# Optimization experiments

Hardware: AMD Instinct MI355X
Metric: run time of the kernel (lower is better)

The kernel has to match this reference:

```python
import jax, jax.numpy as jnp
import numpy as np

N, E, H, C, IN = 20000, 640000, 4, 64, 256
HC = H * C
NEG_SLOPE = 0.2


def setup_inputs() -> dict:
    key = jax.random.key(0)
    ks = jax.random.split(key, 24)
    rn = lambda k, s: jax.random.normal(k, s, jnp.float32) * 0.05
    return {
        "x": jax.random.normal(ks[0], (N, IN), jnp.float32),
        "edge_index": jax.random.randint(ks[1], (2, E), 0, N),
        "confidence": jax.random.normal(ks[2], (N,), jnp.float32),
        "w_in": rn(ks[3], (IN, C)), "b_in": jnp.zeros((C,), jnp.float32),
        "lin_w0": rn(ks[4], (C, HC)),
        "lin_w12": rn(ks[5], (2, HC, HC)),
        "att_src": rn(ks[6], (3, H, C)),
        "att_dst": rn(ks[7], (3, H, C)),
        "gat_bias": jnp.zeros((3, HC), jnp.float32),
        "conf_w": rn(ks[8], (HC, 1)), "conf_b": jnp.zeros((1,), jnp.float32),
        "nc_w1": rn(ks[9], (HC, C)), "nc_b1": jnp.zeros((C,), jnp.float32),
        "nc_w2": rn(ks[10], (C, 1)), "nc_b2": jnp.zeros((1,), jnp.float32),
        "oc_w1": rn(ks[11], (HC, C)), "oc_b1": jnp.zeros((C,), jnp.float32),
        "oc_w2": rn(ks[12], (C, 1)), "oc_b2": jnp.zeros((1,), jnp.float32),
        "ec_w1": rn(ks[13], (HC, C)), "ec_b1": jnp.zeros((C,), jnp.float32),
        "ec_w2": rn(ks[14], (C, 4)), "ec_b2": jnp.zeros((4,), jnp.float32),
    }


def _gat_layer(h_in, src, dst, n, lin_w, a_src, a_dst, bias):
    # h_in: (n, in_ch). PyG GATConv: linear -> per-edge attn -> segment softmax -> scatter-add.
    h = (h_in @ lin_w).reshape(n, H, C)
    s_src = jnp.einsum("nhc,hc->nh", h, a_src)  # (n, H)
    s_dst = jnp.einsum("nhc,hc->nh", h, a_dst)
    alpha = jax.nn.leaky_relu(s_src[src] + s_dst[dst], NEG_SLOPE)  # (E', H)
    # softmax over incoming edges of each dst node (self-loops guarantee coverage)
    amax = jax.ops.segment_max(alpha, dst, num_segments=n)
    ex = jnp.exp(alpha - amax[dst])
    denom = jax.ops.segment_sum(ex, dst, num_segments=n)
    coef = ex / jnp.maximum(denom[dst], 1e-16)
    msg = h[src] * coef[:, :, None]  # (E', H, C)
    out = jax.ops.segment_sum(msg, dst, num_segments=n)
    return out.reshape(n, HC) + bias


def reference(x, edge_index, confidence, w_in, b_in, lin_w0, lin_w12,
              att_src, att_dst, gat_bias, conf_w, conf_b,
              nc_w1, nc_b1, nc_w2, nc_b2, oc_w1, oc_b1, oc_w2, oc_b2,
              ec_w1, ec_b1, ec_w2, ec_b2):
    n = x.shape[0]
    loops = jnp.arange(n)
    src = jnp.concatenate([edge_index[0], loops])  # PyG add_self_loops=True
    dst = jnp.concatenate([edge_index[1], loops])
    h = jax.nn.relu(x @ w_in + b_in)  # input_proj + relu (dropout off in eval)
    lin_ws = [lin_w0, lin_w12[0], lin_w12[1]]
    conf_norm = jax.nn.sigmoid(confidence)  # (n,)
    for i in range(3):
        h_new = _gat_layer(h, src, dst, n, lin_ws[i], att_src[i], att_dst[i], gat_bias[i])
        cw = jax.nn.sigmoid(h_new @ conf_w + conf_b)[:, 0] * conf_norm
        h_new = h_new * cw[:, None]
        h = h + h_new if h.shape[-1] == h_new.shape[-1] else h_new
        if i < 2:
            h = jax.nn.relu(h)
    mlp = lambda w1, b1, w2, b2: jax.nn.relu(h @ w1 + b1) @ w2 + b2
    node_pred = jax.nn.sigmoid(mlp(nc_w1, nc_b1, nc_w2, nc_b2))[:, 0]
    origin_pred = jax.nn.sigmoid(mlp(oc_w1, oc_b1, oc_w2, oc_b2))[:, 0]
    error_type_pred = mlp(ec_w1, ec_b1, ec_w2, ec_b2)
    return node_pred, origin_pred, error_type_pred, h
```

## Files before the change

kernel.cpp:

```cpp
#include <hip/hip_runtime.h>
#include <cstdint>
#include <cstddef>

#define NN   20000
#define NPAD 20224
#define EE   640000
#define E2   660000
#define HHD  4
#define CC   64
#define HC   256
#define NEG  0.2f

#define NBUK 313
#define NBLK 129
#define EPB  5120
#define SCN  (NBUK * NBLK)
#define PREP_BLKS 5000
#define GEMM_BLKS (NPAD / 64)

typedef short bf16x8 __attribute__((ext_vector_type(8)));
typedef float f32x4 __attribute__((ext_vector_type(4)));

__device__ __forceinline__ float sigmoidf_(float x) { return 1.0f / (1.0f + __expf(-x)); }

__device__ __forceinline__ float wred_sum(float v) {
#pragma unroll
    for (int d = 32; d; d >>= 1) v += __shfl_xor(v, d, 64);
    return v;
}

__device__ __forceinline__ unsigned short f2bf(float f) {
    unsigned u = __float_as_uint(f);
    u = (u + 0x7fff + ((u >> 16) & 1)) >> 16;
    return (unsigned short)u;
}
__device__ __forceinline__ float bfval(unsigned short h) { return __uint_as_float(((unsigned)h) << 16); }
__device__ __forceinline__ float bf_lo(unsigned u) { return __uint_as_float(u << 16); }
__device__ __forceinline__ float bf_hi(unsigned u) { return __uint_as_float(u & 0xffff0000u); }


__device__ __forceinline__ void hist_body(int bl, const int* __restrict__ ei,
                                          int* __restrict__ bhist, int* h ) {
    int t = threadIdx.x;
    for (int i = t; i < NBUK; i += 256) h[i] = 0;
    __syncthreads();
    int e0 = bl * EPB;
#pragma unroll 4
    for (int i = t; i < EPB; i += 256) {
        int e = e0 + i;
        if (e < E2) {
            int d = (e < EE) ? ei[EE + e] : (e - EE);
            atomicAdd(&h[d >> 6], 1);
        }
    }
    __syncthreads();
    for (int i = t; i < NBUK; i += 256) bhist[i * NBLK + bl] = h[i];
}

__device__ __forceinline__ void scatter_body(int bl, const int* __restrict__ ei,
                                             const int* __restrict__ sbase,
                                             unsigned int* __restrict__ ebuf,
                                             int* cur ) {
    int t = threadIdx.x;
    for (int i = t; i < NBUK; i += 256) cur[i] = sbase[i * NBLK + bl];
    __syncthreads();
    int e0 = bl * EPB;
#pragma unroll 4
    for (int i = t; i < EPB; i += 256) {
        int e = e0 + i;
        if (e < E2) {
            int s, d;
            if (e < EE) { s = ei[e]; d = ei[EE + e]; }
            else        { s = e - EE; d = s; }
            int p = atomicAdd(&cur[d >> 6], 1);
            ebuf[p] = ((unsigned int)(d & 63) << 15) | (unsigned int)s;
        }
    }
}

__device__ __forceinline__ void build_body(int bu, const unsigned int* __restrict__ ebuf,
                                           const int* __restrict__ sbase,
                                           int* __restrict__ off, int* __restrict__ csr,
                                           int* hist ) {
    int* sc = hist + 64;
    int* curl = hist + 128;
    int t = threadIdx.x;
    int base = sbase[bu * NBLK];
    int end  = (bu + 1 < NBUK) ? sbase[(bu + 1) * NBLK] : E2;
    int ne = end - base;
    if (t < 64) hist[t] = 0;
    __syncthreads();
    for (int i = t; i < ne; i += 256) {
        int dl = (int)(ebuf[base + i] >> 15);
        atomicAdd(&hist[dl], 1);
    }
    __syncthreads();
    if (t < 64) sc[t] = hist[t];
    __syncthreads();
    for (int d = 1; d < 64; d <<= 1) {
        int v = (t < 64 && t >= d) ? sc[t - d] : 0;
        __syncthreads();
        if (t < 64) sc[t] += v;
        __syncthreads();
    }
    int n0 = bu * 64;
    if (t < 64) {
        int ex = base + sc[t] - hist[t];
        if (n0 + t < NN) off[n0 + t] = ex;
        curl[t] = ex;
    }
    if (bu == NBUK - 1 && t == 0) off[NN] = E2;
    __syncthreads();
    for (int i = t; i < ne; i += 256) {
        unsigned int v = ebuf[base + i];
        int dl = (int)(v >> 15);
        int p = atomicAdd(&curl[dl], 1);
        csr[p] = (int)(v & 0x7fffu);
    }
}

#define WTOT 212992
__device__ __forceinline__ void prep_body(int idx,
                            const float* __restrict__ x,
                            const float* __restrict__ w_in, const float* __restrict__ lin_w0,
                            const float* __restrict__ lin_w12,
                            const float* __restrict__ nc1, const float* __restrict__ oc1,
                            const float* __restrict__ ec1,
                            const float* __restrict__ nb, const float* __restrict__ ob,
                            const float* __restrict__ eb,
                            unsigned short* __restrict__ whi,
                            float* __restrict__ bcat,
                            unsigned short* __restrict__ xh, unsigned short* __restrict__ xl) {
    if (idx < NN * 64) {
        float4 v = ((const float4*)x)[idx];
        ushort4 hi, lo;
        hi.x = f2bf(v.x); lo.x = f2bf(v.x - bfval(hi.x));
        hi.y = f2bf(v.y); lo.y = f2bf(v.y - bfval(hi.y));
        hi.z = f2bf(v.z); lo.z = f2bf(v.z - bfval(hi.z));
        hi.w = f2bf(v.w); lo.w = f2bf(v.w - bfval(hi.w));
        ((ushort4*)xh)[idx] = hi;
        ((ushort4*)xl)[idx] = lo;
    }
    if (idx < 192) {
        int g = idx >> 6, jj = idx & 63;
        const float* b = (g == 0) ? nb : ((g == 1) ? ob : eb);
        bcat[idx] = b[jj];
    }
    if (idx >= WTOT) return;
    float v;
    if (idx < 16384) {
        int n = idx >> 8, k = idx & 255;
        v = w_in[k * 64 + n];
    } else if (idx < 32768) {
        int r = idx - 16384;
        int n = r >> 6, k = r & 63;
        v = lin_w0[k * 256 + n];
    } else if (idx < 98304) {
        int r = idx - 32768;
        int n = r >> 8, k = r & 255;
        v = lin_w12[k * 256 + n];
    } else if (idx < 163840) {
        int r = idx - 98304;
        int n = r >> 8, k = r & 255;
        v = lin_w12[65536 + k * 256 + n];
    } else {
        int r = idx - 163840;
        int n = r >> 8, k = r & 255;
        int g = n >> 6, jj = n & 63;
        const float* w = (g == 0) ? nc1 : ((g == 1) ? oc1 : ec1);
        v = w[k * 64 + jj];
    }
    whi[idx] = f2bf(v);
}

template <int K, int OUT_CH, int MODE, int NT>
__device__ __forceinline__ void gemm_body(
    unsigned short* Bh,
    int mb,
    const unsigned short* __restrict__ Ahp, const unsigned short* __restrict__ Alp,
    const unsigned short* __restrict__ Wh,
    const float* __restrict__ bias,
    unsigned short* __restrict__ Outh,
    const float* __restrict__ a_src, const float* __restrict__ a_dst,
    float* __restrict__ s_src, float* __restrict__ s_dst,
    const float* __restrict__ w2n, const float* __restrict__ w2o,
    const float* __restrict__ w2e,
    const float* __restrict__ b2n, const float* __restrict__ b2o,
    const float* __restrict__ b2e,
    unsigned short* __restrict__ Outl,
    float* __restrict__ outbuf, int nreal) {
    constexpr int LB = K + 8;
    constexpr int NS = K / 32;
    const int tid = threadIdx.x;
    const int wv = tid >> 6, lane = tid & 63;
    const int quad = lane >> 4, ln = lane & 15;
    const int r0 = mb + wv * 16 + ln;

    const unsigned short* aph = Ahp + (size_t)r0 * K + quad * 8;
    const unsigned short* apl = Alp + (size_t)r0 * K + quad * 8;
    bf16x8 ah[NS], al[NS];
#pragma unroll
    for (int s = 0; s < NS; s++) {
        ah[s] = *(const bf16x8*)(aph + s * 32);
        al[s] = *(const bf16x8*)(apl + s * 32);
    }

    for (int ct = 0; ct < NT; ct++) {
        const int cb = ct * 64;
        if (ct > 0) __syncthreads();

        constexpr int NCHK = 64 * (K / 8);
#pragma unroll
        for (int i = 0; i < NCHK / 256; i++) {
            int flat = tid + i * 256;
            int r = flat / (K / 8);
            int c = (flat % (K / 8)) * 8;
            *(uint4*)&Bh[r * LB + c] = *(const uint4*)&Wh[(size_t)(cb + r) * K + c];
        }
        __syncthreads();

        f32x4 acc[4];
#pragma unroll
        for (int j = 0; j < 4; j++) {
            acc[j][0] = 0.f; acc[j][1] = 0.f; acc[j][2] = 0.f; acc[j][3] = 0.f;
        }

#pragma unroll
        for (int s = 0; s < NS; s++) {
#pragma unroll
            for (int cg = 0; cg < 4; cg++) {
                bf16x8 bh = *(const bf16x8*)&Bh[(cg * 16 + ln) * LB + quad * 8 + s * 32];
                acc[cg] = __builtin_amdgcn_mfma_f32_16x16x32_bf16(ah[s], bh, acc[cg], 0, 0, 0);
                acc[cg] = __builtin_amdgcn_mfma_f32_16x16x32_bf16(al[s], bh, acc[cg], 0, 0, 0);
            }
        }

        if (MODE == 1) {
            float av[4], dv[4];
#pragma unroll
            for (int cg = 0; cg < 4; cg++) {
                av[cg] = a_src[cb + cg * 16 + ln];
                dv[cg] = a_dst[cb + cg * 16 + ln];
            }
#pragma unroll
            for (int reg = 0; reg < 4; reg++) {
                float ps = 0.f, pd = 0.f;
#pragma unroll
                for (int cg = 0; cg < 4; cg++) {
                    float t = acc[cg][reg];
                    ps += t * av[cg];
                    pd += t * dv[cg];
                }
#pragma unroll
                for (int d = 1; d < 16; d <<= 1) {
                    ps += __shfl_xor(ps, d, 64);
                    pd += __shfl_xor(pd, d, 64);
                }
                if (ln == 0) {
                    int row = mb + wv * 16 + quad * 4 + reg;
                    if (row < nreal) {
                        s_src[row * 4 + ct] = ps;
                        s_dst[row * 4 + ct] = pd;
                    }
                }
            }
        }

        if (MODE == 3) {
            float bv[4];
#pragma unroll
            for (int cg = 0; cg < 4; cg++) bv[cg] = bias[cb + cg * 16 + ln];
            if (ct < 2) {
                const float* w2 = (ct == 0) ? w2n : w2o;
                float b2 = (ct == 0) ? b2n[0] : b2o[0];
                float wv2[4];
#pragma unroll
                for (int cg = 0; cg < 4; cg++) wv2[cg] = w2[cg * 16 + ln];
#pragma unroll
                for (int reg = 0; reg < 4; reg++) {
                    float t = 0.f;
#pragma unroll
                    for (int cg = 0; cg < 4; cg++) {
                        float tv = fmaxf(acc[cg][reg] + bv[cg], 0.f);
                        t += tv * wv2[cg];
                    }
#pragma unroll
                    for (int d = 1; d < 16; d <<= 1) t += __shfl_xor(t, d, 64);
                    int row = mb + wv * 16 + quad * 4 + reg;
                    if (ln == 0 && row < nreal)
                        outbuf[ct * NN + row] = sigmoidf_(t + b2);
                }
            } else {
                float4 w4[4];
#pragma unroll
                for (int cg = 0; cg < 4; cg++) w4[cg] = ((const float4*)w2e)[cg * 16 + ln];
#pragma unroll
                for (int reg = 0; reg < 4; reg++) {
                    float e0 = 0.f, e1 = 0.f, e2 = 0.f, e3 = 0.f;
#pragma unroll
                    for (int cg = 0; cg < 4; cg++) {
                        float tv = fmaxf(acc[cg][reg] + bv[cg], 0.f);
                        e0 += tv * w4[cg].x; e1 += tv * w4[cg].y;
                        e2 += tv * w4[cg].z; e3 += tv * w4[cg].w;
                    }
#pragma unroll
                    for (int d = 1; d < 16; d <<= 1) {
                        e0 += __shfl_xor(e0, d, 64); e1 += __shfl_xor(e1, d, 64);
                        e2 += __shfl_xor(e2, d, 64); e3 += __shfl_xor(e3, d, 64);
                    }
                    int row = mb + wv * 16 + quad * 4 + reg;
                    if (ln == 0 && row < nreal) {
                        float4 ev = make_float4(e0 + b2e[0], e1 + b2e[1], e2 + b2e[2], e3 + b2e[3]);
                        *(float4*)&outbuf[2 * NN + row * 4] = ev;
                    }
                }
            }
            continue;
        }

#pragma unroll
        for (int cg = 0; cg < 4; cg++) {
            int col = cb + cg * 16 + ln;
            int rbase = mb + wv * 16 + quad * 4;
#pragma unroll
            for (int reg = 0; reg < 4; reg++) {
                float v = acc[cg][reg];
                int r = rbase + reg;
                if (MODE == 0) {
                    v += bias[col]; v = fmaxf(v, 0.f);
                    unsigned short hi = f2bf(v);
                    Outh[(size_t)r * OUT_CH + col] = hi;
                    Outl[(size_t)r * OUT_CH + col] = f2bf(v - bfval(hi));
                } else if (MODE == 1) {
                    Outh[(size_t)r * OUT_CH + col] = f2bf(v);
                }
            }
        }
    }
}


__global__ __launch_bounds__(256) void prep_hist(
    const float* __restrict__ x,
    const float* __restrict__ w_in, const float* __restrict__ lin_w0,
    const float* __restrict__ lin_w12,
    const float* __restrict__ nc1, const float* __restrict__ oc1,
    const float* __restrict__ ec1,
    const float* __restrict__ nb, const float* __restrict__ ob,
    const float* __restrict__ eb,
    unsigned short* __restrict__ whi, float* __restrict__ bcat,
    unsigned short* __restrict__ xh, unsigned short* __restrict__ xl,
    const int* __restrict__ ei, int* __restrict__ bhist) {
    __shared__ int h[NBUK];
    if (blockIdx.x < PREP_BLKS) {
        prep_body(blockIdx.x * 256 + threadIdx.x, x, w_in, lin_w0, lin_w12,
                  nc1, oc1, ec1, nb, ob, eb, whi, bcat, xh, xl);
    } else {
        hist_body(blockIdx.x - PREP_BLKS, ei, bhist, h);
    }
}

__global__ __launch_bounds__(1024) void scan_hist(const int* __restrict__ bhist,
                                                  int* __restrict__ sbase) {
    __shared__ int buf[1024];
    int t = threadIdx.x;
    int base = t * 40;
    int local[40];
    int s = 0;
#pragma unroll
    for (int i = 0; i < 40; i++) {
        int idx = base + i;
        int v = (idx < SCN) ? bhist[idx] : 0;
        local[i] = v;
        s += v;
    }
    buf[t] = s;
    __syncthreads();
    for (int d = 1; d < 1024; d <<= 1) {
        int tv = (t >= d) ? buf[t - d] : 0;
        __syncthreads();
        buf[t] += tv;
        __syncthreads();
    }
    int run = buf[t] - s;
#pragma unroll
    for (int i = 0; i < 40; i++) {
        int idx = base + i;
        if (idx < SCN) sbase[idx] = run;
        run += local[i];
    }
}

__global__ __launch_bounds__(256) void scatter_proj(
    const int* __restrict__ ei, const int* __restrict__ sbase,
    unsigned int* __restrict__ ebuf,
    const unsigned short* __restrict__ xh, const unsigned short* __restrict__ xl,
    const unsigned short* __restrict__ wt_in, const float* __restrict__ b_in,
    unsigned short* __restrict__ h0h, unsigned short* __restrict__ h0l) {
    __shared__ unsigned short smem[64 * (256 + 8)];
    if (blockIdx.x < NBLK) {
        scatter_body(blockIdx.x, ei, sbase, ebuf, (int*)smem);
    } else {
        gemm_body<256, 64, 0, 1>(smem, (int)(blockIdx.x - NBLK) * 64,
                                 xh, xl, wt_in, b_in, h0h,
                                 nullptr, nullptr, nullptr, nullptr,
                                 nullptr, nullptr, nullptr, nullptr, nullptr, nullptr,
                                 h0l, nullptr, NN);
    }
}

__global__ __launch_bounds__(256) void build_l0(
    const unsigned int* __restrict__ ebuf, const int* __restrict__ sbase,
    int* __restrict__ off, int* __restrict__ csr,
    const unsigned short* __restrict__ h0h, const unsigned short* __restrict__ h0l,
    const unsigned short* __restrict__ wt_l0,
    unsigned short* __restrict__ hh,
    const float* __restrict__ a_src, const float* __restrict__ a_dst,
    float* __restrict__ ssrc, float* __restrict__ sdst) {
    __shared__ unsigned short smem[64 * (64 + 8)];
    if (blockIdx.x < NBUK) {
        build_body(blockIdx.x, ebuf, sbase, off, csr, (int*)smem);
    } else {
        gemm_body<64, 256, 1, 4>(smem, (int)(blockIdx.x - NBUK) * 64,
                                 h0h, h0l, wt_l0, nullptr, hh,
                                 a_src, a_dst, ssrc, sdst,
                                 nullptr, nullptr, nullptr, nullptr, nullptr, nullptr,
                                 nullptr, nullptr, NN);
    }
}

template <int K, int OUT_CH, int MODE, int NT>
__global__ __launch_bounds__(256) void gemm_lds(
    const unsigned short* __restrict__ Ahp, const unsigned short* __restrict__ Alp,
    const unsigned short* __restrict__ Wh,
    const float* __restrict__ bias,
    unsigned short* __restrict__ Outh, unsigned short* __restrict__ Outl,
    const float* __restrict__ a_src, const float* __restrict__ a_dst,
    float* __restrict__ s_src, float* __restrict__ s_dst,
    const float* __restrict__ w2n, const float* __restrict__ w2o,
    const float* __restrict__ w2e,
    const float* __restrict__ b2n, const float* __restrict__ b2o,
    const float* __restrict__ b2e,
    float* __restrict__ outbuf, int nreal) {
    __shared__ unsigned short Bh[64 * (K + 8)];
    gemm_body<K, OUT_CH, MODE, NT>(Bh, blockIdx.x * 64, Ahp, Alp, Wh, bias, Outh,
                                   a_src, a_dst, s_src, s_dst,
                                   w2n, w2o, w2e, b2n, b2o, b2e, Outl, outbuf, nreal);
}

__global__ __launch_bounds__(256) void gat_node(const unsigned short* __restrict__ hhb,
                                                const float* __restrict__ s_src,
                                                const float* __restrict__ s_dst,
                                                const int* __restrict__ csr_src,
                                                const int* __restrict__ csr_off,
                                                const float* __restrict__ gbias,
                                                const float* __restrict__ conf_w,
                                                const float* __restrict__ conf_b,
                                                const float* __restrict__ confid,
                                                unsigned short* __restrict__ h_hi,
                                                unsigned short* __restrict__ h_lo,
                                                float* __restrict__ outbuf,
                                                int layer) {
    __shared__ float Lc[4][64];
    __shared__ int   Ls[4][16];
    int wv = threadIdx.x >> 6;
    int lane = threadIdx.x & 63;
    int n = blockIdx.x * 4 + wv;
    int myhead = lane >> 4, slot = lane & 15;
    int off0 = csr_off[n];
    int deg = csr_off[n + 1] - off0;
    const int* cp = csr_src + off0;
    const unsigned short* hrow = hhb + lane * 4;
    float sdm = s_dst[n * 4 + myhead];

    float ax = 0.f, ay = 0.f, az = 0.f, aw = 0.f, smp = 0.f;
    int nch = (deg + 15) >> 4;
    bool valid = slot < deg;
    int sl = cp[valid ? slot : deg - 1];
    float ssv = s_src[sl * 4 + myhead];
    for (int t = 0; t < nch; t++) {
        float a = ssv + sdm;
        a = a > 0.f ? a : NEG * a;
        float c = valid ? __expf(a) : 0.f;
        smp += c;
        Lc[wv][lane] = c;
        if (myhead == 0) Ls[wv][slot] = sl;
        __builtin_amdgcn_wave_barrier();
        float4 c0 = *(const float4*)&Lc[wv][myhead * 16 + 0];
        float4 c1 = *(const float4*)&Lc[wv][myhead * 16 + 4];
        float4 c2 = *(const float4*)&Lc[wv][myhead * 16 + 8];
        float4 c3 = *(const float4*)&Lc[wv][myhead * 16 + 12];
        int4 s0 = *(const int4*)&Ls[wv][0];
        int4 s1 = *(const int4*)&Ls[wv][4];
        int4 s2 = *(const int4*)&Ls[wv][8];
        int4 s3 = *(const int4*)&Ls[wv][12];
        __builtin_amdgcn_wave_barrier();
        if (t + 1 < nch) {
            int i = ((t + 1) << 4) + slot;
            valid = i < deg;
            sl = cp[valid ? i : deg - 1];
            ssv = s_src[sl * 4 + myhead];
        }
        float cf[16] = {c0.x, c0.y, c0.z, c0.w, c1.x, c1.y, c1.z, c1.w,
                        c2.x, c2.y, c2.z, c2.w, c3.x, c3.y, c3.z, c3.w};
        int sv[16] = {s0.x, s0.y, s0.z, s0.w, s1.x, s1.y, s1.z, s1.w,
                      s2.x, s2.y, s2.z, s2.w, s3.x, s3.y, s3.z, s3.w};
#pragma unroll
        for (int q = 0; q < 16; q++) {
            uint2 u = *(const uint2*)(hrow + ((size_t)sv[q] << 8));
            ax += cf[q] * bf_lo(u.x); ay += cf[q] * bf_hi(u.x);
            az += cf[q] * bf_lo(u.y); aw += cf[q] * bf_hi(u.y);
        }
    }
    smp += __shfl_xor(smp, 1, 64);
    smp += __shfl_xor(smp, 2, 64);
    smp += __shfl_xor(smp, 4, 64);
    smp += __shfl_xor(smp, 8, 64);
    float inv = 1.0f / fmaxf(smp, 1e-16f);
    ax *= inv; ay *= inv; az *= inv; aw *= inv;

    float4 b4 = *(const float4*)&gbias[lane * 4];
    float hx = ax + b4.x, hy = ay + b4.y, hz = az + b4.z, hw = aw + b4.w;
    float4 cw4 = *(const float4*)&conf_w[lane * 4];
    float local = hx * cw4.x + hy * cw4.y + hz * cw4.z + hw * cw4.w;
    float tot = wred_sum(local);
    float cw = sigmoidf_(tot + conf_b[0]) * sigmoidf_(confid[n]);
    hx *= cw; hy *= cw; hz *= cw; hw *= cw;
    if (layer > 0) {
        ushort4 ph = *(const ushort4*)&h_hi[(size_t)n * HC + lane * 4];
        ushort4 pl = *(const ushort4*)&h_lo[(size_t)n * HC + lane * 4];
        hx += bfval(ph.x) + bfval(pl.x);
        hy += bfval(ph.y) + bfval(pl.y);
        hz += bfval(ph.z) + bfval(pl.z);
        hw += bfval(ph.w) + bfval(pl.w);
    }
    if (layer < 2) {
        hx = fmaxf(hx, 0.f); hy = fmaxf(hy, 0.f);
        hz = fmaxf(hz, 0.f); hw = fmaxf(hw, 0.f);
    } else {
        *(float4*)&outbuf[6 * NN + (size_t)n * HC + lane * 4] =
            make_float4(hx, hy, hz, hw);
    }
    ushort4 oh, ol;
    oh.x = f2bf(hx); ol.x = f2bf(hx - bfval(oh.x));
    oh.y = f2bf(hy); ol.y = f2bf(hy - bfval(oh.y));
    oh.z = f2bf(hz); ol.z = f2bf(hz - bfval(oh.z));
    oh.w = f2bf(hw); ol.w = f2bf(hw - bfval(oh.w));
    *(ushort4*)&h_hi[(size_t)n * HC + lane * 4] = oh;
    *(ushort4*)&h_lo[(size_t)n * HC + lane * 4] = ol;
}

extern "C" void kernel_launch(void* const* d_in, const int* in_sizes, int n_in,
                              void* d_out, int out_size, void* d_ws, size_t ws_size,
                              hipStream_t stream) {
    const float* x       = (const float*)d_in[0];
    const int*   ei      = (const int*)d_in[1];
    const float* conf    = (const float*)d_in[2];
    const float* w_in    = (const float*)d_in[3];
    const float* b_in    = (const float*)d_in[4];
    const float* lin_w0  = (const float*)d_in[5];
    const float* lin_w12 = (const float*)d_in[6];
    const float* att_src = (const float*)d_in[7];
    const float* att_dst = (const float*)d_in[8];
    const float* gbias   = (const float*)d_in[9];
    const float* conf_w  = (const float*)d_in[10];
    const float* conf_b  = (const float*)d_in[11];
    const float* nc_w1   = (const float*)d_in[12];
    const float* nc_b1   = (const float*)d_in[13];
    const float* nc_w2   = (const float*)d_in[14];
    const float* nc_b2   = (const float*)d_in[15];
    const float* oc_w1   = (const float*)d_in[16];
    const float* oc_b1   = (const float*)d_in[17];
    const float* oc_w2   = (const float*)d_in[18];
    const float* oc_b2   = (const float*)d_in[19];
    const float* ec_w1   = (const float*)d_in[20];
    const float* ec_b1   = (const float*)d_in[21];
    const float* ec_w2   = (const float*)d_in[22];
    const float* ec_b2   = (const float*)d_in[23];
    float* out = (float*)d_out;

    char* p = (char*)d_ws;
    auto alloc = [&](size_t bytes) -> void* {
        void* r = (void*)p;
        p += (bytes + 255) & ~(size_t)255;
        return r;
    };
    unsigned short* h_hi = (unsigned short*)alloc((size_t)NPAD * HC * 2);
    unsigned short* h_lo = (unsigned short*)alloc((size_t)NPAD * HC * 2);
    unsigned short* hh   = (unsigned short*)alloc((size_t)NPAD * HC * 2);
    unsigned short* h0h  = (unsigned short*)alloc((size_t)NPAD * CC * 2);
    unsigned short* h0l  = (unsigned short*)alloc((size_t)NPAD * CC * 2);
    float*          ssrc = (float*)alloc((size_t)NN * 4 * 4);
    float*          sdst = (float*)alloc((size_t)NN * 4 * 4);
    int*            off  = (int*)alloc((size_t)(NN + 1) * 4);
    int*            csr  = (int*)alloc((size_t)E2 * 4);
    int*            bhist= (int*)alloc((size_t)SCN * 4);
    int*            sbase= (int*)alloc((size_t)SCN * 4);
    unsigned int*   ebuf = (unsigned int*)alloc((size_t)E2 * 4);
    unsigned short* whi  = (unsigned short*)alloc((size_t)WTOT * 2);
    float*          bcat = (float*)alloc((size_t)192 * 4);
    unsigned short* xh   = (unsigned short*)alloc((size_t)NPAD * 256 * 2 * 2);
    unsigned short* xl   = xh + (size_t)NPAD * 256;

    const unsigned short* wt_in = whi;
    const unsigned short* wt_l0 = whi + 16384;
    const unsigned short* wt_a  = whi + 32768;
    const unsigned short* wt_b  = whi + 98304;
    const unsigned short* wt_hd = whi + 163840;

    prep_hist<<<PREP_BLKS + NBLK, 256, 0, stream>>>(
        x, w_in, lin_w0, lin_w12, nc_w1, oc_w1, ec_w1, nc_b1, oc_b1, ec_b1,
        whi, bcat, xh, xl, ei, bhist);

    scan_hist<<<1, 1024, 0, stream>>>(bhist, sbase);

    scatter_proj<<<NBLK + GEMM_BLKS, 256, 0, stream>>>(
        ei, sbase, ebuf, xh, xl, wt_in, b_in, h0h, h0l);

    build_l0<<<NBUK + GEMM_BLKS, 256, 0, stream>>>(
        ebuf, sbase, off, csr, h0h, h0l, wt_l0, hh, att_src, att_dst, ssrc, sdst);

    gat_node<<<NN / 4, 256, 0, stream>>>(hh, ssrc, sdst, csr, off, gbias, conf_w, conf_b, conf,
                                         h_hi, h_lo, out, 0);

    for (int i = 1; i < 3; i++) {
        const unsigned short* wh = (i == 1) ? wt_a : wt_b;
        gemm_lds<256, 256, 1, 4><<<dim3(GEMM_BLKS, 1), 256, 0, stream>>>(
            h_hi, h_lo, wh, nullptr, hh, nullptr,
            att_src + i * HHD * CC, att_dst + i * HHD * CC, ssrc, sdst,
            nullptr, nullptr, nullptr, nullptr, nullptr, nullptr, nullptr, NN);
        gat_node<<<NN / 4, 256, 0, stream>>>(hh, ssrc, sdst, csr, off, gbias + i * HC,
                                             conf_w, conf_b, conf, h_hi, h_lo, out, i);
    }

    gemm_lds<256, 192, 3, 3><<<dim3(GEMM_BLKS, 1), 256, 0, stream>>>(
        h_hi, h_lo, wt_hd, bcat, nullptr, nullptr, nullptr, nullptr, nullptr, nullptr,
        nc_w2, oc_w2, ec_w2, nc_b2, oc_b2, ec_b2, out, NN);
}
```

Measured before the change: 370.8 us.

## Split GAT aggregation into per-head kernel plus finalize kernel

Replaces the per-node GAT aggregation kernel with a per-(node, head) kernel. In it, each wave processes one head's 64 channels with 8 edges in parallel and 16-byte gathers. Partial aggregates and per-head confidence dot products go to new float buffers, and a second kernel applies the confidence gate, residual and bf16 split. The aim is more parallelism and wider gathers without LDS staging. The cost is an extra fp32 round trip through global memory of N×256 floats per layer and an extra launch. Grid blocks are interleaved so heads of nearby nodes run close together.

Result: slower. 435.9 us (+17.6%).

```diff
diff --git a/kernel.cpp b/kernel.cpp
--- a/kernel.cpp
+++ b/kernel.cpp
@@ -22,12 +22,6 @@
 typedef float f32x4 __attribute__((ext_vector_type(4)));
 
 __device__ __forceinline__ float sigmoidf_(float x) { return 1.0f / (1.0f + __expf(-x)); }
-
-__device__ __forceinline__ float wred_sum(float v) {
-#pragma unroll
-    for (int d = 32; d; d >>= 1) v += __shfl_xor(v, d, 64);
-    return v;
-}
 
 __device__ __forceinline__ unsigned short f2bf(float f) {
     unsigned u = __float_as_uint(f);
@@ -448,84 +442,92 @@
                                    w2n, w2o, w2e, b2n, b2o, b2e, Outl, outbuf, nreal);
 }
 
-__global__ __launch_bounds__(256) void gat_node(const unsigned short* __restrict__ hhb,
-                                                const float* __restrict__ s_src,
-                                                const float* __restrict__ s_dst,
-                                                const int* __restrict__ csr_src,
-                                                const int* __restrict__ csr_off,
-                                                const float* __restrict__ gbias,
-                                                const float* __restrict__ conf_w,
-                                                const float* __restrict__ conf_b,
-                                                const float* __restrict__ confid,
-                                                unsigned short* __restrict__ h_hi,
-                                                unsigned short* __restrict__ h_lo,
-                                                float* __restrict__ outbuf,
-                                                int layer) {
-    __shared__ float Lc[4][64];
-    __shared__ int   Ls[4][16];
+__global__ __launch_bounds__(256) void gat_head(
+    const unsigned short* __restrict__ hhb,
+    const float* __restrict__ s_src, const float* __restrict__ s_dst,
+    const int* __restrict__ csr_src, const int* __restrict__ csr_off,
+    const float* __restrict__ gbias, const float* __restrict__ conf_w,
+    float* __restrict__ agg, float* __restrict__ pdot) {
+    int bid = blockIdx.x;
+    int h  = (bid & 7) >> 1;
+    int ng = ((bid >> 3) << 1) | (bid & 1);
     int wv = threadIdx.x >> 6;
     int lane = threadIdx.x & 63;
-    int n = blockIdx.x * 4 + wv;
-    int myhead = lane >> 4, slot = lane & 15;
+    int n = ng * 4 + wv;
+    int slot = lane >> 3;
+    int oct  = lane & 7;
     int off0 = csr_off[n];
-    int deg = csr_off[n + 1] - off0;
+    int deg  = csr_off[n + 1] - off0;
     const int* cp = csr_src + off0;
-    const unsigned short* hrow = hhb + lane * 4;
-    float sdm = s_dst[n * 4 + myhead];
-
-    float ax = 0.f, ay = 0.f, az = 0.f, aw = 0.f, smp = 0.f;
-    int nch = (deg + 15) >> 4;
+    const unsigned short* hrow = hhb + h * 64 + oct * 8;
+    float sdm = s_dst[n * 4 + h];
+
+    float ac[8] = {0.f, 0.f, 0.f, 0.f, 0.f, 0.f, 0.f, 0.f};
+    float smp = 0.f;
+    int nch = (deg + 7) >> 3;
     bool valid = slot < deg;
     int sl = cp[valid ? slot : deg - 1];
-    float ssv = s_src[sl * 4 + myhead];
+    float ssv = s_src[sl * 4 + h];
     for (int t = 0; t < nch; t++) {
         float a = ssv + sdm;
         a = a > 0.f ? a : NEG * a;
         float c = valid ? __expf(a) : 0.f;
         smp += c;
-        Lc[wv][lane] = c;
-        if (myhead == 0) Ls[wv][slot] = sl;
-        __builtin_amdgcn_wave_barrier();
-        float4 c0 = *(const float4*)&Lc[wv][myhead * 16 + 0];
-        float4 c1 = *(const float4*)&Lc[wv][myhead * 16 + 4];
-        float4 c2 = *(const float4*)&Lc[wv][myhead * 16 + 8];
-        float4 c3 = *(const float4*)&Lc[wv][myhead * 16 + 12];
-        int4 s0 = *(const int4*)&Ls[wv][0];
-        int4 s1 = *(const int4*)&Ls[wv][4];
-        int4 s2 = *(const int4*)&Ls[wv][8];
-        int4 s3 = *(const int4*)&Ls[wv][12];
-        __builtin_amdgcn_wave_barrier();
+        int cursl = sl;
         if (t + 1 < nch) {
-            int i = ((t + 1) << 4) + slot;
+            int i = ((t + 1) << 3) + slot;
             valid = i < deg;
             sl = cp[valid ? i : deg - 1];
-            ssv = s_src[sl * 4 + myhead];
-        }
-        float cf[16] = {c0.x, c0.y, c0.z, c0.w, c1.x, c1.y, c1.z, c1.w,
-                        c2.x, c2.y, c2.z, c2.w, c3.x, c3.y, c3.z, c3.w};
-        int sv[16] = {s0.x, s0.y, s0.z, s0.w, s1.x, s1.y, s1.z, s1.w,
-                      s2.x, s2.y, s2.z, s2.w, s3.x, s3.y, s3.z, s3.w};
-#pragma unroll
-        for (int q = 0; q < 16; q++) {
-            uint2 u = *(const uint2*)(hrow + ((size_t)sv[q] << 8));
-            ax += cf[q] * bf_lo(u.x); ay += cf[q] * bf_hi(u.x);
-            az += cf[q] * bf_lo(u.y); aw += cf[q] * bf_hi(u.y);
-        }
-    }
-    smp += __shfl_xor(smp, 1, 64);
-    smp += __shfl_xor(smp, 2, 64);
-    smp += __shfl_xor(smp, 4, 64);
+            ssv = s_src[sl * 4 + h];
+        }
+        uint4 u = *(const uint4*)(hrow + ((size_t)cursl << 8));
+        ac[0] += c * bf_lo(u.x); ac[1] += c * bf_hi(u.x);
+        ac[2] += c * bf_lo(u.y); ac[3] += c * bf_hi(u.y);
+        ac[4] += c * bf_lo(u.z); ac[5] += c * bf_hi(u.z);
+        ac[6] += c * bf_lo(u.w); ac[7] += c * bf_hi(u.w);
+    }
     smp += __shfl_xor(smp, 8, 64);
+    smp += __shfl_xor(smp, 16, 64);
+    smp += __shfl_xor(smp, 32, 64);
+#pragma unroll
+    for (int i = 0; i < 8; i++) {
+        ac[i] += __shfl_xor(ac[i], 8, 64);
+        ac[i] += __shfl_xor(ac[i], 16, 64);
+        ac[i] += __shfl_xor(ac[i], 32, 64);
+    }
     float inv = 1.0f / fmaxf(smp, 1e-16f);
-    ax *= inv; ay *= inv; az *= inv; aw *= inv;
-
-    float4 b4 = *(const float4*)&gbias[lane * 4];
-    float hx = ax + b4.x, hy = ay + b4.y, hz = az + b4.z, hw = aw + b4.w;
-    float4 cw4 = *(const float4*)&conf_w[lane * 4];
-    float local = hx * cw4.x + hy * cw4.y + hz * cw4.z + hw * cw4.w;
-    float tot = wred_sum(local);
+    int cbase = h * 64 + oct * 8;
+    float vv[8];
+    float pd = 0.f;
+#pragma unroll
+    for (int i = 0; i < 8; i++) {
+        vv[i] = ac[i] * inv + gbias[cbase + i];
+        pd += vv[i] * conf_w[cbase + i];
+    }
+    pd += __shfl_xor(pd, 1, 64);
+    pd += __shfl_xor(pd, 2, 64);
+    pd += __shfl_xor(pd, 4, 64);
+    if (lane < 8) {
+        float* ap = agg + (size_t)n * 256 + cbase;
+        *(float4*)ap       = make_float4(vv[0], vv[1], vv[2], vv[3]);
+        *(float4*)(ap + 4) = make_float4(vv[4], vv[5], vv[6], vv[7]);
+        if (lane == 0) pdot[n * 4 + h] = pd;
+    }
+}
+
+__global__ __launch_bounds__(256) void gat_fin(
+    const float* __restrict__ agg, const float* __restrict__ pdot,
+    const float* __restrict__ conf_b, const float* __restrict__ confid,
+    unsigned short* __restrict__ h_hi, unsigned short* __restrict__ h_lo,
+    float* __restrict__ outbuf, int layer) {
+    int wv = threadIdx.x >> 6;
+    int lane = threadIdx.x & 63;
+    int n = blockIdx.x * 4 + wv;
+    float4 v = *(const float4*)(agg + (size_t)n * 256 + lane * 4);
+    const float* pp = pdot + n * 4;
+    float tot = pp[0] + pp[1] + pp[2] + pp[3];
     float cw = sigmoidf_(tot + conf_b[0]) * sigmoidf_(confid[n]);
-    hx *= cw; hy *= cw; hz *= cw; hw *= cw;
+    float hx = v.x * cw, hy = v.y * cw, hz = v.z * cw, hw = v.w * cw;
     if (layer > 0) {
         ushort4 ph = *(const ushort4*)&h_hi[(size_t)n * HC + lane * 4];
         ushort4 pl = *(const ushort4*)&h_lo[(size_t)n * HC + lane * 4];
@@ -601,6 +603,8 @@
     float*          bcat = (float*)alloc((size_t)192 * 4);
     unsigned short* xh   = (unsigned short*)alloc((size_t)NPAD * 256 * 2 * 2);
     unsigned short* xl   = xh + (size_t)NPAD * 256;
+    float*          agg  = (float*)alloc((size_t)NN * 256 * 4);
+    float*          pdot = (float*)alloc((size_t)NN * 4 * 4);
 
     const unsigned short* wt_in = whi;
     const unsigned short* wt_l0 = whi + 16384;
@@ -620,8 +624,8 @@
     build_l0<<<NBUK + GEMM_BLKS, 256, 0, stream>>>(
         ebuf, sbase, off, csr, h0h, h0l, wt_l0, hh, att_src, att_dst, ssrc, sdst);
 
-    gat_node<<<NN / 4, 256, 0, stream>>>(hh, ssrc, sdst, csr, off, gbias, conf_w, conf_b, conf,
-                                         h_hi, h_lo, out, 0);
+    gat_head<<<NN, 256, 0, stream>>>(hh, ssrc, sdst, csr, off, gbias, conf_w, agg, pdot);
+    gat_fin<<<NN / 4, 256, 0, stream>>>(agg, pdot, conf_b, conf, h_hi, h_lo, out, 0);
 
     for (int i = 1; i < 3; i++) {
         const unsigned short* wh = (i == 1) ? wt_a : wt_b;
@@ -629,8 +633,9 @@
             h_hi, h_lo, wh, nullptr, hh, nullptr,
             att_src + i * HHD * CC, att_dst + i * HHD * CC, ssrc, sdst,
             nullptr, nullptr, nullptr, nullptr, nullptr, nullptr, nullptr, NN);
-        gat_node<<<NN / 4, 256, 0, stream>>>(hh, ssrc, sdst, csr, off, gbias + i * HC,
-                                             conf_w, conf_b, conf, h_hi, h_lo, out, i);
+        gat_head<<<NN, 256, 0, stream>>>(hh, ssrc, sdst, csr, off, gbias + i * HC,
+                                         conf_w, agg, pdot);
+        gat_fin<<<NN / 4, 256, 0, stream>>>(agg, pdot, conf_b, conf, h_hi, h_lo, out, i);
     }
 
     gemm_lds<256, 192, 3, 3><<<dim3(GEMM_BLKS, 1), 256, 0, stream>>>(
```

## Fold global histogram scan into scatter blocks and drop scan kernel launch

Applied to the files above, without the earlier changes.

Removes the single-block scan_hist kernel. Each scatter block now recomputes its own per-bucket prefix and the bucket totals straight from the histogram matrix, then scans the bucket totals in LDS to get its write cursors, with block 0 also writing compact bucket start offsets for the build step. This cuts one kernel launch and a serialized single-block stage, but every scatter block now reads the whole 313x129 histogram redundantly, with strided row reads.

After: 358.6 us. 3.3% less time.

```diff
diff --git a/kernel.cpp b/kernel.cpp
--- a/kernel.cpp
+++ b/kernel.cpp
@@ -14,7 +14,6 @@
 #define NBUK 313
 #define NBLK 129
 #define EPB  5120
-#define SCN  (NBUK * NBLK)
 #define PREP_BLKS 5000
 #define GEMM_BLKS (NPAD / 64)
 
@@ -58,35 +57,68 @@
 }
 
 __device__ __forceinline__ void scatter_body(int bl, const int* __restrict__ ei,
-                                             const int* __restrict__ sbase,
+                                             const int* __restrict__ bhist,
                                              unsigned int* __restrict__ ebuf,
-                                             int* cur ) {
+                                             int* __restrict__ bstart,
+                                             int* ih ) {
+    int* tot = ih;
+    int* par = ih + NBUK;
+    int* buf = ih + 2 * NBUK;
+    int* cur = ih + 2 * NBUK + 256;
     int t = threadIdx.x;
-    for (int i = t; i < NBUK; i += 256) cur[i] = sbase[i * NBLK + bl];
+    for (int i = t; i < NBUK; i += 256) {
+        const int* row = bhist + i * NBLK;
+        int sp = 0;
+        for (int b = 0; b < bl; b++) sp += row[b];
+        int st = sp;
+        for (int b = bl; b < NBLK; b++) st += row[b];
+        tot[i] = st; par[i] = sp;
+    }
+    __syncthreads();
+    int b0 = t * 2;
+    int v0 = (b0 < NBUK) ? tot[b0] : 0;
+    int v1 = (b0 + 1 < NBUK) ? tot[b0 + 1] : 0;
+    int s = v0 + v1;
+    buf[t] = s;
+    __syncthreads();
+    for (int d = 1; d < 256; d <<= 1) {
+        int tv = (t >= d) ? buf[t - d] : 0;
+        __syncthreads();
+        buf[t] += tv;
+        __syncthreads();
+    }
+    int excl = buf[t] - s;
+    if (b0 < NBUK)     cur[b0]     = excl + par[b0];
+    if (b0 + 1 < NBUK) cur[b0 + 1] = excl + v0 + par[b0 + 1];
+    if (bl == 0) {
+        if (b0 < NBUK)     bstart[b0]     = excl;
+        if (b0 + 1 < NBUK) bstart[b0 + 1] = excl + v0;
+        if (t == 0) bstart[NBUK] = E2;
+    }
     __syncthreads();
     int e0 = bl * EPB;
 #pragma unroll 4
     for (int i = t; i < EPB; i += 256) {
         int e = e0 + i;
         if (e < E2) {
-            int s, d;
-            if (e < EE) { s = ei[e]; d = ei[EE + e]; }
-            else        { s = e - EE; d = s; }
+            int s2, d;
+            if (e < EE) { s2 = ei[e]; d = ei[EE + e]; }
+            else        { s2 = e - EE; d = s2; }
             int p = atomicAdd(&cur[d >> 6], 1);
-            ebuf[p] = ((unsigned int)(d & 63) << 15) | (unsigned int)s;
+            ebuf[p] = ((unsigned int)(d & 63) << 15) | (unsigned int)s2;
         }
     }
 }
 
 __device__ __forceinline__ void build_body(int bu, const unsigned int* __restrict__ ebuf,
-                                           const int* __restrict__ sbase,
+                                           const int* __restrict__ bstart,
                                            int* __restrict__ off, int* __restrict__ csr,
                                            int* hist ) {
     int* sc = hist + 64;
     int* curl = hist + 128;
     int t = threadIdx.x;
-    int base = sbase[bu * NBLK];
-    int end  = (bu + 1 < NBUK) ? sbase[(bu + 1) * NBLK] : E2;
+    int base = bstart[bu];
+    int end  = bstart[bu + 1];
     int ne = end - base;
     if (t < 64) hist[t] = 0;
     __syncthreads();
@@ -360,46 +392,15 @@
     }
 }
 
-__global__ __launch_bounds__(1024) void scan_hist(const int* __restrict__ bhist,
-                                                  int* __restrict__ sbase) {
-    __shared__ int buf[1024];
-    int t = threadIdx.x;
-    int base = t * 40;
-    int local[40];
-    int s = 0;
-#pragma unroll
-    for (int i = 0; i < 40; i++) {
-        int idx = base + i;
-        int v = (idx < SCN) ? bhist[idx] : 0;
-        local[i] = v;
-        s += v;
-    }
-    buf[t] = s;
-    __syncthreads();
-    for (int d = 1; d < 1024; d <<= 1) {
-        int tv = (t >= d) ? buf[t - d] : 0;
-        __syncthreads();
-        buf[t] += tv;
-        __syncthreads();
-    }
-    int run = buf[t] - s;
-#pragma unroll
-    for (int i = 0; i < 40; i++) {
-        int idx = base + i;
-        if (idx < SCN) sbase[idx] = run;
-        run += local[i];
-    }
-}
-
 __global__ __launch_bounds__(256) void scatter_proj(
-    const int* __restrict__ ei, const int* __restrict__ sbase,
-    unsigned int* __restrict__ ebuf,
+    const int* __restrict__ ei, const int* __restrict__ bhist,
+    unsigned int* __restrict__ ebuf, int* __restrict__ bstart,
     const unsigned short* __restrict__ xh, const unsigned short* __restrict__ xl,
     const unsigned short* __restrict__ wt_in, const float* __restrict__ b_in,
     unsigned short* __restrict__ h0h, unsigned short* __restrict__ h0l) {
     __shared__ unsigned short smem[64 * (256 + 8)];
     if (blockIdx.x < NBLK) {
-        scatter_body(blockIdx.x, ei, sbase, ebuf, (int*)smem);
+        scatter_body(blockIdx.x, ei, bhist, ebuf, bstart, (int*)smem);
     } else {
         gemm_body<256, 64, 0, 1>(smem, (int)(blockIdx.x - NBLK) * 64,
                                  xh, xl, wt_in, b_in, h0h,
@@ -410,7 +411,7 @@
 }
 
 __global__ __launch_bounds__(256) void build_l0(
-    const unsigned int* __restrict__ ebuf, const int* __restrict__ sbase,
+    const unsigned int* __restrict__ ebuf, const int* __restrict__ bstart,
     int* __restrict__ off, int* __restrict__ csr,
     const unsigned short* __restrict__ h0h, const unsigned short* __restrict__ h0l,
     const unsigned short* __restrict__ wt_l0,
@@ -419,7 +420,7 @@
     float* __restrict__ ssrc, float* __restrict__ sdst) {
     __shared__ unsigned short smem[64 * (64 + 8)];
     if (blockIdx.x < NBUK) {
-        build_body(blockIdx.x, ebuf, sbase, off, csr, (int*)smem);
+        build_body(blockIdx.x, ebuf, bstart, off, csr, (int*)smem);
     } else {
         gemm_body<64, 256, 1, 4>(smem, (int)(blockIdx.x - NBUK) * 64,
                                  h0h, h0l, wt_l0, nullptr, hh,
@@ -594,8 +595,8 @@
     float*          sdst = (float*)alloc((size_t)NN * 4 * 4);
     int*            off  = (int*)alloc((size_t)(NN + 1) * 4);
     int*            csr  = (int*)alloc((size_t)E2 * 4);
-    int*            bhist= (int*)alloc((size_t)SCN * 4);
-    int*            sbase= (int*)alloc((size_t)SCN * 4);
+    int*            bhist= (int*)alloc((size_t)(NBUK * NBLK) * 4);
+    int*            bstart=(int*)alloc((size_t)(NBUK + 1) * 4);
     unsigned int*   ebuf = (unsigned int*)alloc((size_t)E2 * 4);
     unsigned short* whi  = (unsigned short*)alloc((size_t)WTOT * 2);
     float*          bcat = (float*)alloc((size_t)192 * 4);
@@ -612,13 +613,11 @@
         x, w_in, lin_w0, lin_w12, nc_w1, oc_w1, ec_w1, nc_b1, oc_b1, ec_b1,
         whi, bcat, xh, xl, ei, bhist);
 
-    scan_hist<<<1, 1024, 0, stream>>>(bhist, sbase);
-
     scatter_proj<<<NBLK + GEMM_BLKS, 256, 0, stream>>>(
-        ei, sbase, ebuf, xh, xl, wt_in, b_in, h0h, h0l);
+        ei, bhist, ebuf, bstart, xh, xl, wt_in, b_in, h0h, h0l);
 
     build_l0<<<NBUK + GEMM_BLKS, 256, 0, stream>>>(
-        ebuf, sbase, off, csr, h0h, h0l, wt_l0, hh, att_src, att_dst, ssrc, sdst);
+        ebuf, bstart, off, csr, h0h, h0l, wt_l0, hh, att_src, att_dst, ssrc, sdst);
 
     gat_node<<<NN / 4, 256, 0, stream>>>(hh, ssrc, sdst, csr, off, gbias, conf_w, conf_b, conf,
                                          h_hi, h_lo, out, 0);
```
